# Optimization experiments

Measured on AMD Instinct MI355X. Metric: run time of the kernel, lower is better.

Reference implementation:

```python
import jax, jax.numpy as jnp
import numpy as np

N = 1_000_000
D = 64      # input_size
O = 64      # output_size


def setup_inputs() -> dict:
    key = jax.random.key(0)
    k1, k2, k3, k4, k5 = jax.random.split(key, 5)
    x = jax.random.normal(k1, (N, D), dtype=jnp.float32)
    item_to_left_idxs = jax.random.randint(k2, (N,), 0, N, dtype=jnp.int64 if jax.config.jax_enable_x64 else jnp.int32)
    item_to_right_idxs = jax.random.randint(k3, (N,), 0, N, dtype=jnp.int64 if jax.config.jax_enable_x64 else jnp.int32)
    # nn.Linear(3*D, O): weight [O, 3*D], bias [O]
    bound = 1.0 / np.sqrt(3 * D)
    W = jax.random.uniform(k4, (O, 3 * D), dtype=jnp.float32, minval=-bound, maxval=bound)
    b = jax.random.uniform(k5, (O,), dtype=jnp.float32, minval=-bound, maxval=bound)
    return {"x": x, "item_to_left_idxs": item_to_left_idxs,
            "item_to_right_idxs": item_to_right_idxs, "W": W, "b": b}


def reference(x, item_to_left_idxs, item_to_right_idxs, W, b):
    # cat((x, x[left], x[right]), -1) @ W.T + b
    # Expressed as three smaller GEMMs on the weight slices to avoid
    # materializing the [N, 3D] concat (same math as the torch module).
    Wx, Wl, Wr = W[:, :D], W[:, D:2 * D], W[:, 2 * D:]
    out = (jnp.einsum('nd,od->no', x, Wx)
           + jnp.einsum('nd,od->no', x[item_to_left_idxs], Wl)
           + jnp.einsum('nd,od->no', x[item_to_right_idxs], Wr)
           + b)
    return out
```

## Files before the change

kernel.cpp:

```cpp
#include <hip/hip_runtime.h>


typedef __bf16 bf16x8 __attribute__((ext_vector_type(8)));
typedef float floatx4 __attribute__((ext_vector_type(4)));

#define D 64
#define O 64
#define K3 192

__global__ __launch_bounds__(256) void polyconv_kernel(
    const float* __restrict__ x,
    const int* __restrict__ lidx,
    const int* __restrict__ ridx,
    const float* __restrict__ W,
    const float* __restrict__ bias,
    float* __restrict__ out,
    int n_tiles, int total_waves)
{
    const int lane = threadIdx.x & 63;
    const int wave_id = blockIdx.x * (blockDim.x >> 6) + (threadIdx.x >> 6);
    const int col  = lane & 15;
    const int quad = lane >> 4;

    bf16x8 bfrag[6][4];
#pragma unroll
    for (int ct = 0; ct < 4; ++ct) {
        const float* wrow = W + (size_t)(ct * 16 + col) * K3 + quad * 8;
#pragma unroll
        for (int ks = 0; ks < 6; ++ks) {
            floatx4 w0 = *(const floatx4*)(wrow + ks * 32);
            floatx4 w1 = *(const floatx4*)(wrow + ks * 32 + 4);
            bf16x8 f;
            f[0] = (__bf16)w0[0]; f[1] = (__bf16)w0[1];
            f[2] = (__bf16)w0[2]; f[3] = (__bf16)w0[3];
            f[4] = (__bf16)w1[0]; f[5] = (__bf16)w1[1];
            f[6] = (__bf16)w1[2]; f[7] = (__bf16)w1[3];
            bfrag[ks][ct] = f;
        }
    }
    float bi[4];
#pragma unroll
    for (int ct = 0; ct < 4; ++ct) bi[ct] = bias[ct * 16 + col];

    for (int t = wave_id; t < n_tiles; t += total_waves) {
        const int base = t * 16;
        const int item = base + col;
        const int li = lidx[item];
        const int ri = ridx[item];
        const float* px = x + (size_t)item * D + quad * 8;
        const float* pl = x + (size_t)li   * D + quad * 8;
        const float* pr = x + (size_t)ri   * D + quad * 8;
        floatx4 v[12];
        v[0]  = *(const floatx4*)(px);      v[1]  = *(const floatx4*)(px + 4);
        v[2]  = *(const floatx4*)(px + 32); v[3]  = *(const floatx4*)(px + 36);
        v[4]  = *(const floatx4*)(pl);      v[5]  = *(const floatx4*)(pl + 4);
        v[6]  = *(const floatx4*)(pl + 32); v[7]  = *(const floatx4*)(pl + 36);
        v[8]  = *(const floatx4*)(pr);      v[9]  = *(const floatx4*)(pr + 4);
        v[10] = *(const floatx4*)(pr + 32); v[11] = *(const floatx4*)(pr + 36);

        bf16x8 afrag[6];
#pragma unroll
        for (int ks = 0; ks < 6; ++ks) {
            floatx4 a0 = v[2 * ks], a1 = v[2 * ks + 1];
            bf16x8 f;
            f[0] = (__bf16)a0[0]; f[1] = (__bf16)a0[1];
            f[2] = (__bf16)a0[2]; f[3] = (__bf16)a0[3];
            f[4] = (__bf16)a1[0]; f[5] = (__bf16)a1[1];
            f[6] = (__bf16)a1[2]; f[7] = (__bf16)a1[3];
            afrag[ks] = f;
        }

        floatx4 acc[4];
#pragma unroll
        for (int ct = 0; ct < 4; ++ct) acc[ct] = (floatx4){0.f, 0.f, 0.f, 0.f};
#pragma unroll
        for (int ct = 0; ct < 4; ++ct)
#pragma unroll
            for (int ks = 0; ks < 6; ++ks)
                acc[ct] = __builtin_amdgcn_mfma_f32_16x16x32_bf16(
                    afrag[ks], bfrag[ks][ct], acc[ct], 0, 0, 0);

        float* orow = out + (size_t)base * O;
#pragma unroll
        for (int ct = 0; ct < 4; ++ct) {
#pragma unroll
            for (int r = 0; r < 4; ++r) {
                int m = quad * 4 + r;
                __builtin_nontemporal_store(acc[ct][r] + bi[ct],
                                            orow + (size_t)m * O + ct * 16 + col);
            }
        }
    }
}

extern "C" void kernel_launch(void* const* d_in, const int* in_sizes, int n_in,
                              void* d_out, int out_size, void* d_ws, size_t ws_size,
                              hipStream_t stream) {
    const float* x  = (const float*)d_in[0];
    const int*   li = (const int*)d_in[1];
    const int*   ri = (const int*)d_in[2];
    const float* W  = (const float*)d_in[3];
    const float* b  = (const float*)d_in[4];
    float* out = (float*)d_out;

    const int n = in_sizes[1];
    const int n_tiles = n / 16;
    const int blocks = 1024;
    const int total_waves = blocks * 4;
    polyconv_kernel<<<blocks, 256, 0, stream>>>(x, li, ri, W, b, out,
                                                n_tiles, total_waves);
}
```

Measured before the change: 525.3 us.

## Double-buffer gathers with index prefetch and halve the grid

Restructures the persistent tile loop into a two-stage software pipeline. Each iteration issues the row gathers for the next tile and prefetches the indices for the tile after that before running MFMA and stores on the current tile, so memory latency overlaps compute. The bias is folded into the accumulator initialization. The grid is halved to 512 blocks and launch bounds now request 2 blocks per CU, while the doubled register buffers raise register pressure and may reduce resident waves.

```diff
diff --git a/kernel.cpp b/kernel.cpp
--- a/kernel.cpp
+++ b/kernel.cpp
@@ -8,7 +8,58 @@
 #define O 64
 #define K3 192
 
-__global__ __launch_bounds__(256) void polyconv_kernel(
+__device__ __forceinline__ void issue_gather(floatx4 (&v)[12], const float* __restrict__ x,
+                                             int item, int li, int ri, int quad) {
+    const float* px = x + (size_t)item * D + quad * 8;
+    const float* pl = x + (size_t)li   * D + quad * 8;
+    const float* pr = x + (size_t)ri   * D + quad * 8;
+    v[0]  = *(const floatx4*)(px);      v[1]  = *(const floatx4*)(px + 4);
+    v[2]  = *(const floatx4*)(px + 32); v[3]  = *(const floatx4*)(px + 36);
+    v[4]  = *(const floatx4*)(pl);      v[5]  = *(const floatx4*)(pl + 4);
+    v[6]  = *(const floatx4*)(pl + 32); v[7]  = *(const floatx4*)(pl + 36);
+    v[8]  = *(const floatx4*)(pr);      v[9]  = *(const floatx4*)(pr + 4);
+    v[10] = *(const floatx4*)(pr + 32); v[11] = *(const floatx4*)(pr + 36);
+}
+
+__device__ __forceinline__ void compute_store(const floatx4 (&v)[12],
+                                              const bf16x8 (&bfrag)[6][4],
+                                              const float (&bi)[4],
+                                              float* __restrict__ out,
+                                              int base, int col, int quad) {
+    bf16x8 afrag[6];
+#pragma unroll
+    for (int ks = 0; ks < 6; ++ks) {
+        floatx4 a0 = v[2 * ks], a1 = v[2 * ks + 1];
+        bf16x8 f;
+        f[0] = (__bf16)a0[0]; f[1] = (__bf16)a0[1];
+        f[2] = (__bf16)a0[2]; f[3] = (__bf16)a0[3];
+        f[4] = (__bf16)a1[0]; f[5] = (__bf16)a1[1];
+        f[6] = (__bf16)a1[2]; f[7] = (__bf16)a1[3];
+        afrag[ks] = f;
+    }
+    floatx4 acc[4];
+#pragma unroll
+    for (int ct = 0; ct < 4; ++ct)
+        acc[ct] = (floatx4){bi[ct], bi[ct], bi[ct], bi[ct]};
+#pragma unroll
+    for (int ct = 0; ct < 4; ++ct)
+#pragma unroll
+        for (int ks = 0; ks < 6; ++ks)
+            acc[ct] = __builtin_amdgcn_mfma_f32_16x16x32_bf16(
+                afrag[ks], bfrag[ks][ct], acc[ct], 0, 0, 0);
+
+    float* orow = out + (size_t)base * O;
+#pragma unroll
+    for (int ct = 0; ct < 4; ++ct)
+#pragma unroll
+        for (int r = 0; r < 4; ++r) {
+            int m = quad * 4 + r;
+            __builtin_nontemporal_store(acc[ct][r],
+                                        orow + (size_t)m * O + ct * 16 + col);
+        }
+}
+
+__global__ __launch_bounds__(256, 2) void polyconv_kernel(
     const float* __restrict__ x,
     const int* __restrict__ lidx,
     const int* __restrict__ ridx,
@@ -42,54 +93,39 @@
 #pragma unroll
     for (int ct = 0; ct < 4; ++ct) bi[ct] = bias[ct * 16 + col];
 
-    for (int t = wave_id; t < n_tiles; t += total_waves) {
-        const int base = t * 16;
-        const int item = base + col;
-        const int li = lidx[item];
-        const int ri = ridx[item];
-        const float* px = x + (size_t)item * D + quad * 8;
-        const float* pl = x + (size_t)li   * D + quad * 8;
-        const float* pr = x + (size_t)ri   * D + quad * 8;
-        floatx4 v[12];
-        v[0]  = *(const floatx4*)(px);      v[1]  = *(const floatx4*)(px + 4);
-        v[2]  = *(const floatx4*)(px + 32); v[3]  = *(const floatx4*)(px + 36);
-        v[4]  = *(const floatx4*)(pl);      v[5]  = *(const floatx4*)(pl + 4);
-        v[6]  = *(const floatx4*)(pl + 32); v[7]  = *(const floatx4*)(pl + 36);
-        v[8]  = *(const floatx4*)(pr);      v[9]  = *(const floatx4*)(pr + 4);
-        v[10] = *(const floatx4*)(pr + 32); v[11] = *(const floatx4*)(pr + 36);
+    const int stride = total_waves;
+    int t = wave_id;
+    if (t >= n_tiles) return;
 
-        bf16x8 afrag[6];
-#pragma unroll
-        for (int ks = 0; ks < 6; ++ks) {
-            floatx4 a0 = v[2 * ks], a1 = v[2 * ks + 1];
-            bf16x8 f;
-            f[0] = (__bf16)a0[0]; f[1] = (__bf16)a0[1];
-            f[2] = (__bf16)a0[2]; f[3] = (__bf16)a0[3];
-            f[4] = (__bf16)a1[0]; f[5] = (__bf16)a1[1];
-            f[6] = (__bf16)a1[2]; f[7] = (__bf16)a1[3];
-            afrag[ks] = f;
+    floatx4 va[12], vb[12];
+    int li_n = 0, ri_n = 0;
+
+    {
+        int item = t * 16 + col;
+        int li = lidx[item], ri = ridx[item];
+        issue_gather(va, x, item, li, ri, quad);
+    }
+    int t1 = t + stride;
+    if (t1 < n_tiles) { li_n = lidx[t1 * 16 + col]; ri_n = ridx[t1 * 16 + col]; }
+
+    while (true) {
+        if (t1 < n_tiles) {
+            issue_gather(vb, x, t1 * 16 + col, li_n, ri_n, quad);
+            int t2 = t1 + stride;
+            if (t2 < n_tiles) { li_n = lidx[t2 * 16 + col]; ri_n = ridx[t2 * 16 + col]; }
         }
+        compute_store(va, bfrag, bi, out, t * 16, col, quad);
+        t = t1; t1 += stride;
+        if (t >= n_tiles) break;
 
-        floatx4 acc[4];
-#pragma unroll
-        for (int ct = 0; ct < 4; ++ct) acc[ct] = (floatx4){0.f, 0.f, 0.f, 0.f};
-#pragma unroll
-        for (int ct = 0; ct < 4; ++ct)
-#pragma unroll
-            for (int ks = 0; ks < 6; ++ks)
-                acc[ct] = __builtin_amdgcn_mfma_f32_16x16x32_bf16(
-                    afrag[ks], bfrag[ks][ct], acc[ct], 0, 0, 0);
-
-        float* orow = out + (size_t)base * O;
-#pragma unroll
-        for (int ct = 0; ct < 4; ++ct) {
-#pragma unroll
-            for (int r = 0; r < 4; ++r) {
-                int m = quad * 4 + r;
-                __builtin_nontemporal_store(acc[ct][r] + bi[ct],
-                                            orow + (size_t)m * O + ct * 16 + col);
-            }
+        if (t1 < n_tiles) {
+            issue_gather(va, x, t1 * 16 + col, li_n, ri_n, quad);
+            int t2 = t1 + stride;
+            if (t2 < n_tiles) { li_n = lidx[t2 * 16 + col]; ri_n = ridx[t2 * 16 + col]; }
         }
+        compute_store(vb, bfrag, bi, out, t * 16, col, quad);
+        t = t1; t1 += stride;
+        if (t >= n_tiles) break;
     }
 }
 
@@ -105,7 +141,7 @@
 
     const int n = in_sizes[1];
     const int n_tiles = n / 16;
-    const int blocks = 1024;
+    const int blocks = 512;
     const int total_waves = blocks * 4;
     polyconv_kernel<<<blocks, 256, 0, stream>>>(x, li, ri, W, b, out,
                                                 n_tiles, total_waves);
```

Result: no change. 515.9 us (-1.8%).
